# Kernel tuning notes

Measured on AMD Instinct MI355X. Metric: run time of the kernel, lower is better.

The kernel has to match this reference:

```python
import jax, jax.numpy as jnp
import numpy as np

B, C, H, W = 8, 128, 48, 48
RED = 16  # SELayer reduction


def setup_inputs() -> dict:
    key = jax.random.key(0)
    ks = jax.random.split(key, 8)
    s = 0.05  # weight scale for numerical stability of softmax
    return {
        "x": jax.random.normal(ks[0], (B, C, H, W), jnp.float32),
        "Wq": jax.random.normal(ks[1], (C, C), jnp.float32) * s,
        "bq": jnp.zeros((C,), jnp.float32),
        "Wk": jax.random.normal(ks[2], (C, C), jnp.float32) * s,
        "bk": jnp.zeros((C,), jnp.float32),
        "Wv": jax.random.normal(ks[3], (C, C), jnp.float32) * s,
        "bv": jnp.zeros((C,), jnp.float32),
        "se_w1": jax.random.normal(ks[4], (C // RED, C), jnp.float32) * s,
        "se_w2": jax.random.normal(ks[5], (C, C // RED), jnp.float32) * s,
        "gamma": jax.random.normal(ks[6], (1,), jnp.float32),
    }


def reference(x, Wq, bq, Wk, bk, Wv, bv, se_w1, se_w2, gamma):
    b, c, h, w = x.shape
    n = h * w
    xf = x.reshape(b, c, n)  # (B, C, N)
    # 1x1 convs == per-pixel linear maps over channels
    q = jnp.einsum('oc,bcn->bon', Wq, xf) + bq[None, :, None]  # (B, C, N)
    k = jnp.einsum('oc,bcn->bon', Wk, xf) + bk[None, :, None]
    v = jnp.einsum('oc,bcn->bon', Wv, xf) + bv[None, :, None]
    # energy[b, i, j] = sum_c q[b, c, i] * k[b, c, j]  (unscaled, as in source)
    energy = jnp.einsum('bci,bcj->bij', q, k)  # (B, N, N)
    attn = jax.nn.softmax(energy, axis=-1)
    # out[b, c, i] = sum_j v[b, c, j] * attn[b, i, j]
    out = jnp.einsum('bcj,bij->bci', v, attn).reshape(b, c, h, w)
    # SELayer applied to the input x
    y = jnp.mean(x, axis=(2, 3))  # (B, C) global average pool
    y = jax.nn.relu(y @ se_w1.T)  # (B, C//RED)
    y = jax.nn.sigmoid(y @ se_w2.T)  # (B, C)
    x_se = x * y[:, :, None, None]
    return gamma[0] * out + x_se
```

## Files before the change

kernel.cpp:

```cpp
#include <hip/hip_runtime.h>

typedef _Float16 half8 __attribute__((ext_vector_type(8)));
typedef _Float16 half4 __attribute__((ext_vector_type(4)));
typedef float f32x4 __attribute__((ext_vector_type(4)));

#define BATCH 8
#define CH 128
#define NPIX 2304
#define SPLIT 6
#define JTILES 6
#define BN (BATCH * NPIX)
#define LOG2E 1.44269504088896f
#define PB2 25.96851f

__device__ __forceinline__ f32x4 mfma32(half8 a, half8 b, f32x4 c) {
    return __builtin_amdgcn_mfma_f32_16x16x32_f16(a, b, c, 0, 0, 0);
}

__global__ __launch_bounds__(256) void k_prep(
        const float* __restrict__ x, const float* __restrict__ Wq,
        const float* __restrict__ Wk, const float* __restrict__ Wv,
        _Float16* __restrict__ Wh, float* __restrict__ y0) {
    const int bid = blockIdx.x;
    const int t = threadIdx.x;
    if (bid < 1024) {
        const int row = bid;
        const float4* p = (const float4*)(x + (size_t)row * NPIX);
        float s = 0.f;
        for (int tt = t; tt < NPIX / 4; tt += 256) {
            float4 v = p[tt];
            s += v.x + v.y + v.z + v.w;
        }
        for (int m = 1; m < 64; m <<= 1) s += __shfl_xor(s, m);
        __shared__ float ls[4];
        if ((t & 63) == 0) ls[t >> 6] = s;
        __syncthreads();
        if (t == 0) y0[row] = (ls[0] + ls[1] + ls[2] + ls[3]) * (1.0f / (float)NPIX);
    } else {
        int i = (bid - 1024) * 256 + t;
        const float* src = (i < 16384) ? Wq : ((i < 32768) ? Wk : Wv);
        Wh[i] = (_Float16)src[i & 16383];
    }
}

__global__ __launch_bounds__(256) void k_proj(
        const float* __restrict__ x, const _Float16* __restrict__ Wh,
        const float* __restrict__ bq, const float* __restrict__ bk, const float* __restrict__ bv,
        _Float16* __restrict__ qT, _Float16* __restrict__ kT, _Float16* __restrict__ vN,
        const float* __restrict__ y0, const float* __restrict__ se_w1,
        const float* __restrict__ se_w2, float* __restrict__ scale) {
    const int t = threadIdx.x;
    if (blockIdx.x == 72) {
        if (blockIdx.y != 0) return;
        __shared__ float ly[128];
        __shared__ float ly1[8];
        for (int b = 0; b < BATCH; ++b) {
            if (t < 128) ly[t] = y0[b * 128 + t];
            __syncthreads();
            if (t < 8) {
                float a = 0.f;
                for (int c = 0; c < 128; ++c) a += se_w1[t * 128 + c] * ly[c];
                ly1[t] = fmaxf(a, 0.f);
            }
            __syncthreads();
            if (t < 128) {
                float a = 0.f;
                for (int r = 0; r < 8; ++r) a += se_w2[t * 8 + r] * ly1[r];
                scale[b * 128 + t] = 1.f / (1.f + __expf(-a));
            }
            __syncthreads();
        }
        return;
    }

    const int n0 = blockIdx.x * 32;
    const int b = blockIdx.y;
    __shared__ __align__(16) _Float16 xt[32 * 128];
    __shared__ __align__(16) _Float16 ob[128 * 32];

    {
        const int c4 = (t & 31) * 4;
        const int nn = (t >> 5) * 4;
        const float* xb = x + (size_t)b * CH * NPIX + n0;
        float4 v0 = *(const float4*)(xb + (size_t)(c4 + 0) * NPIX + nn);
        float4 v1 = *(const float4*)(xb + (size_t)(c4 + 1) * NPIX + nn);
        float4 v2 = *(const float4*)(xb + (size_t)(c4 + 2) * NPIX + nn);
        float4 v3 = *(const float4*)(xb + (size_t)(c4 + 3) * NPIX + nn);
        const float xr[4][4] = {{v0.x, v1.x, v2.x, v3.x}, {v0.y, v1.y, v2.y, v3.y},
                                {v0.z, v1.z, v2.z, v3.z}, {v0.w, v1.w, v2.w, v3.w}};
        for (int i = 0; i < 4; ++i) {
            int n = nn + i;
            half4 h;
            h[0] = (_Float16)xr[i][0]; h[1] = (_Float16)xr[i][1];
            h[2] = (_Float16)xr[i][2]; h[3] = (_Float16)xr[i][3];
            *(half4*)(xt + n * 128 + (((c4 >> 3) ^ (n & 7)) * 8) + (c4 & 4)) = h;
        }
    }
    __syncthreads();

    const int lane = t & 63, w = t >> 6;
    const int ln15 = lane & 15, quad = lane >> 4;
    f32x4 zero4 = {0.f, 0.f, 0.f, 0.f};

    for (int proj = 0; proj < 3; ++proj) {
        const _Float16* W = Wh + proj * 16384;
        const float* bias = (proj == 0) ? bq : ((proj == 1) ? bk : bv);
        f32x4 acc[2][2];
        acc[0][0] = zero4; acc[0][1] = zero4; acc[1][0] = zero4; acc[1][1] = zero4;

        for (int kc = 0; kc < 4; ++kc) {
            half8 bf[2];
            for (int nt = 0; nt < 2; ++nt) {
                int n = nt * 16 + ln15;
                bf[nt] = *(const half8*)(xt + n * 128 + (((kc * 4 + quad) ^ (n & 7)) * 8));
            }
            for (int mt = 0; mt < 2; ++mt) {
                half8 af = *(const half8*)(W + (w * 32 + mt * 16 + ln15) * 128 + kc * 32 + quad * 8);
                acc[mt][0] = mfma32(af, bf[0], acc[mt][0]);
                acc[mt][1] = mfma32(af, bf[1], acc[mt][1]);
            }
        }
        __syncthreads();

        if (proj < 2) {
            for (int mt = 0; mt < 2; ++mt)
                for (int nt = 0; nt < 2; ++nt)
                    for (int r = 0; r < 4; ++r) {
                        int c = w * 32 + mt * 16 + quad * 4 + r;
                        int n = nt * 16 + ln15;
                        ob[n * 128 + (((c >> 3) ^ (n & 7)) * 8) + (c & 7)] =
                            (_Float16)(acc[mt][nt][r] + bias[c]);
                    }
            __syncthreads();
            _Float16* dst = ((proj == 0) ? qT : kT) + ((size_t)b * NPIX + n0) * CH;
            for (int rep = 0; rep < 2; ++rep) {
                int n = rep * 16 + (t >> 4), ch = t & 15;
                *(half8*)(dst + n * CH + ch * 8) =
                    *(const half8*)(ob + n * 128 + ((ch ^ (n & 7)) * 8));
            }
        } else {
            for (int mt = 0; mt < 2; ++mt)
                for (int nt = 0; nt < 2; ++nt)
                    for (int r = 0; r < 4; ++r) {
                        int c = w * 32 + mt * 16 + quad * 4 + r;
                        int n = nt * 16 + ln15;
                        ob[c * 32 + (((n >> 3) ^ (c & 3)) * 8) + (n & 7)] =
                            (_Float16)(acc[mt][nt][r] + bias[c]);
                    }
            __syncthreads();
            _Float16* vb = vN + (size_t)b * CH * NPIX + n0;
            for (int rep = 0; rep < 2; ++rep) {
                int c = rep * 64 + (t >> 2), ch = t & 3;
                *(half8*)(vb + (size_t)c * NPIX + ch * 8) =
                    *(const half8*)(ob + c * 32 + ((ch ^ (c & 3)) * 8));
            }
        }
    }
}

__global__ __launch_bounds__(256, 3) void k_attn(
        const _Float16* __restrict__ qT, const _Float16* __restrict__ kT,
        const _Float16* __restrict__ vN,
        _Float16* __restrict__ o_part, float* __restrict__ g_l) {
    const int i0 = blockIdx.x * 128;
    const int b = blockIdx.y;
    const int split = blockIdx.z;
    const int t = threadIdx.x;
    const int lane = t & 63, w = t >> 6;
    const int ln15 = lane & 15, quad = lane >> 4;

    __shared__ __align__(16) _Float16 sh[24576];
    _Float16* k_s = sh;
    _Float16* v_s = sh + 8192;
    _Float16* p_w = sh + 16384 + w * 2048;

    const int iA = i0 + w * 32 + ln15;
    half8 qfA[4], qfB[4];
    {
        const _Float16* qb = qT + ((size_t)b * NPIX + iA) * CH + quad * 8;
        for (int kc = 0; kc < 4; ++kc) {
            qfA[kc] = *(const half8*)(qb + kc * 32);
            qfB[kc] = *(const half8*)(qb + 16 * CH + kc * 32);
        }
    }

    f32x4 zero4 = {0.f, 0.f, 0.f, 0.f};
    f32x4 osA[8], osB[8];
    for (int ct = 0; ct < 8; ++ct) { osA[ct] = zero4; osB[ct] = zero4; }
    float lA = 0.f, lB = 0.f;

    const _Float16* kb = kT + ((size_t)b * NPIX + split * (JTILES * 64)) * CH;
    const _Float16* vb = vN + (size_t)b * CH * NPIX + split * (JTILES * 64);

    for (int it = 0; it < JTILES; ++it) {
        __syncthreads();
        {
            const _Float16* kk = kb + (size_t)it * 64 * CH;
            for (int rep = 0; rep < 4; ++rep) {
                int row = rep * 16 + (t >> 4), ch = t & 15;
                *(half8*)(k_s + row * 128 + ((ch ^ (row & 7)) * 8)) =
                    *(const half8*)(kk + row * CH + ch * 8);
            }
        }
        {
            const _Float16* vv = vb + it * 64;
            for (int rep = 0; rep < 4; ++rep) {
                int c = rep * 32 + (t >> 3), ch = t & 7;
                *(half8*)(v_s + c * 64 + ((ch ^ (c & 7)) * 8)) =
                    *(const half8*)(vv + (size_t)c * NPIX + ch * 8);
            }
        }
        __syncthreads();

        f32x4 sA[4], sB[4];
        for (int jt = 0; jt < 4; ++jt) { sA[jt] = zero4; sB[jt] = zero4; }
        for (int jt = 0; jt < 4; ++jt) {
            int row = jt * 16 + ln15;
            for (int kc = 0; kc < 4; ++kc) {
                half8 kf = *(const half8*)(k_s + row * 128 + (((kc * 4 + quad) ^ (row & 7)) * 8));
                sA[jt] = mfma32(kf, qfA[kc], sA[jt]);
                sB[jt] = mfma32(kf, qfB[kc], sB[jt]);
            }
        }

        {
            float sum = 0.f;
            for (int jt = 0; jt < 4; ++jt) {
                half4 ph;
                for (int r = 0; r < 4; ++r) {
                    float p = exp2f(fmaf(sA[jt][r], LOG2E, -PB2));
                    sum += p;
                    ph[r] = (_Float16)p;
                }
                *(half4*)(p_w + ln15 * 64 + (((jt * 4 + quad) ^ ln15) * 4)) = ph;
            }
            lA += sum;
        }
        {
            float sum = 0.f;
            for (int jt = 0; jt < 4; ++jt) {
                half4 ph;
                for (int r = 0; r < 4; ++r) {
                    float p = exp2f(fmaf(sB[jt][r], LOG2E, -PB2));
                    sum += p;
                    ph[r] = (_Float16)p;
                }
                *(half4*)(p_w + 1024 + ln15 * 64 + (((jt * 4 + quad) ^ ln15) * 4)) = ph;
            }
            lB += sum;
        }

        for (int t32 = 0; t32 < 2; ++t32) {
            int s0 = t32 * 8 + quad * 2;
            half4 a0 = *(const half4*)(p_w + ln15 * 64 + ((s0 ^ ln15) * 4));
            half4 a1 = *(const half4*)(p_w + ln15 * 64 + (((s0 + 1) ^ ln15) * 4));
            half4 b0 = *(const half4*)(p_w + 1024 + ln15 * 64 + ((s0 ^ ln15) * 4));
            half4 b1 = *(const half4*)(p_w + 1024 + ln15 * 64 + (((s0 + 1) ^ ln15) * 4));
            half8 pfA, pfB;
            for (int e = 0; e < 4; ++e) {
                pfA[e] = a0[e]; pfA[4 + e] = a1[e];
                pfB[e] = b0[e]; pfB[4 + e] = b1[e];
            }
            for (int ct = 0; ct < 8; ++ct) {
                int c = ct * 16 + ln15;
                half8 vf = *(const half8*)(v_s + c * 64 + (((t32 * 4 + quad) ^ (c & 7)) * 8));
                osA[ct] = mfma32(vf, pfA, osA[ct]);
                osB[ct] = mfma32(vf, pfB, osB[ct]);
            }
        }
    }

    lA += __shfl_xor(lA, 16); lA += __shfl_xor(lA, 32);
    lB += __shfl_xor(lB, 16); lB += __shfl_xor(lB, 32);
    if (quad == 0) {
        g_l[(size_t)(split * BATCH + b) * NPIX + iA] = lA;
        g_l[(size_t)(split * BATCH + b) * NPIX + iA + 16] = lB;
    }
    __syncthreads();
    for (int ct = 0; ct < 8; ++ct)
        for (int r = 0; r < 4; ++r) {
            int c = ct * 16 + quad * 4 + r;
            int il = w * 32 + ln15;
            sh[c * 128 + ((((il >> 3) ^ (c & 15)) * 8)) + (il & 7)] = (_Float16)osA[ct][r];
            int il2 = il + 16;
            sh[c * 128 + ((((il2 >> 3) ^ (c & 15)) * 8)) + (il2 & 7)] = (_Float16)osB[ct][r];
        }
    __syncthreads();
    _Float16* opb = o_part + (size_t)(split * BATCH + b) * CH * NPIX;
    for (int rep = 0; rep < 8; ++rep) {
        int c = rep * 16 + (t >> 4), ch = t & 15;
        *(half8*)(opb + (size_t)c * NPIX + i0 + ch * 8) =
            *(const half8*)(sh + c * 128 + ((ch ^ (c & 15)) * 8));
    }
}

__global__ __launch_bounds__(256) void k_combine(
        const _Float16* __restrict__ o_part, const float* __restrict__ g_l,
        const float* __restrict__ x, const float* __restrict__ scale,
        const float* __restrict__ gamma_p, float* __restrict__ out) {
    int tid = blockIdx.x * 256 + threadIdx.x;
    int i8 = (tid % (NPIX / 8)) * 8;
    int bc = tid / (NPIX / 8);
    int b = bc >> 7, c = bc & 127;

    float L[8] = {0.f, 0.f, 0.f, 0.f, 0.f, 0.f, 0.f, 0.f};
    for (int s = 0; s < SPLIT; ++s) {
        const float* lp = g_l + (size_t)(s * BATCH + b) * NPIX + i8;
        float4 la = *(const float4*)(lp);
        float4 lb = *(const float4*)(lp + 4);
        L[0] += la.x; L[1] += la.y; L[2] += la.z; L[3] += la.w;
        L[4] += lb.x; L[5] += lb.y; L[6] += lb.z; L[7] += lb.w;
    }
    float acc[8] = {0.f, 0.f, 0.f, 0.f, 0.f, 0.f, 0.f, 0.f};
    for (int s = 0; s < SPLIT; ++s) {
        half8 o = *(const half8*)(o_part + ((size_t)(s * BATCH + b) * CH + c) * NPIX + i8);
        for (int e = 0; e < 8; ++e) acc[e] += (float)o[e];
    }
    float g = gamma_p[0];
    float sc = scale[bc];
    size_t base = (size_t)bc * NPIX + i8;
    float4 x0 = *(const float4*)(x + base);
    float4 x1 = *(const float4*)(x + base + 4);
    float xv[8] = {x0.x, x0.y, x0.z, x0.w, x1.x, x1.y, x1.z, x1.w};
    float r[8];
    for (int e = 0; e < 8; ++e) r[e] = g * (acc[e] / L[e]) + xv[e] * sc;
    *(float4*)(out + base) = {r[0], r[1], r[2], r[3]};
    *(float4*)(out + base + 4) = {r[4], r[5], r[6], r[7]};
}

extern "C" void kernel_launch(void* const* d_in, const int* in_sizes, int n_in,
                              void* d_out, int out_size, void* d_ws, size_t ws_size,
                              hipStream_t stream) {
    const float* x     = (const float*)d_in[0];
    const float* Wq    = (const float*)d_in[1];
    const float* bq    = (const float*)d_in[2];
    const float* Wk    = (const float*)d_in[3];
    const float* bk    = (const float*)d_in[4];
    const float* Wv    = (const float*)d_in[5];
    const float* bv    = (const float*)d_in[6];
    const float* se_w1 = (const float*)d_in[7];
    const float* se_w2 = (const float*)d_in[8];
    const float* gamma = (const float*)d_in[9];
    float* out = (float*)d_out;

    char* ws = (char*)d_ws;
    const size_t E = (size_t)BATCH * NPIX * CH;
    _Float16* qT = (_Float16*)(ws);
    _Float16* kT = (_Float16*)(ws + E * 2);
    _Float16* vN = (_Float16*)(ws + E * 4);
    _Float16* op = (_Float16*)(ws + E * 6);
    char* tail   = ws + E * 6 + (size_t)SPLIT * E * 2;
    _Float16* Wh = (_Float16*)(tail);
    float* g_l   = (float*)(tail + 98304);
    float* y0    = (float*)(tail + 98304 + (size_t)SPLIT * BN * 4);
    float* scale = (float*)(tail + 98304 + (size_t)SPLIT * BN * 4 + 4096);

    k_prep<<<1216, 256, 0, stream>>>(x, Wq, Wk, Wv, Wh, y0);
    k_proj<<<dim3(73, BATCH), 256, 0, stream>>>(
        x, Wh, bq, bk, bv, qT, kT, vN, y0, se_w1, se_w2, scale);
    k_attn<<<dim3(NPIX / 128, BATCH, SPLIT), 256, 0, stream>>>(
        qT, kT, vN, op, g_l);
    k_combine<<<(int)(E / 8 / 256), 256, 0, stream>>>(
        op, g_l, x, scale, gamma, out);
}
```

Baseline: 178.7 us.

## Fold prep kernel into projection, split attention seven ways, shrink P staging

Removes the separate prep kernel. The global-average-pool sum is now computed inside the projection kernel with atomics, and the weights are converted from fp32 to fp16 on the fly. The SE MLP moves into the combine kernel, which recomputes it per block. Attention is split over 7 uneven j-ranges (6 or 5 tiles each) instead of 6, with smaller per-wave P staging so occupancy can rise to 4 blocks per CU. This trades one fewer launch and a larger grid for atomic contention, redundant SE work, and an extra memset launch.

```diff
diff --git a/kernel.cpp b/kernel.cpp
--- a/kernel.cpp
+++ b/kernel.cpp
@@ -7,8 +7,7 @@
 #define BATCH 8
 #define CH 128
 #define NPIX 2304
-#define SPLIT 6
-#define JTILES 6
+#define NSPLIT 7
 #define BN (BATCH * NPIX)
 #define LOG2E 1.44269504088896f
 #define PB2 25.96851f
@@ -17,64 +16,15 @@
     return __builtin_amdgcn_mfma_f32_16x16x32_f16(a, b, c, 0, 0, 0);
 }
 
-__global__ __launch_bounds__(256) void k_prep(
+__global__ __launch_bounds__(256) void k_proj(
         const float* __restrict__ x, const float* __restrict__ Wq,
         const float* __restrict__ Wk, const float* __restrict__ Wv,
-        _Float16* __restrict__ Wh, float* __restrict__ y0) {
-    const int bid = blockIdx.x;
-    const int t = threadIdx.x;
-    if (bid < 1024) {
-        const int row = bid;
-        const float4* p = (const float4*)(x + (size_t)row * NPIX);
-        float s = 0.f;
-        for (int tt = t; tt < NPIX / 4; tt += 256) {
-            float4 v = p[tt];
-            s += v.x + v.y + v.z + v.w;
-        }
-        for (int m = 1; m < 64; m <<= 1) s += __shfl_xor(s, m);
-        __shared__ float ls[4];
-        if ((t & 63) == 0) ls[t >> 6] = s;
-        __syncthreads();
-        if (t == 0) y0[row] = (ls[0] + ls[1] + ls[2] + ls[3]) * (1.0f / (float)NPIX);
-    } else {
-        int i = (bid - 1024) * 256 + t;
-        const float* src = (i < 16384) ? Wq : ((i < 32768) ? Wk : Wv);
-        Wh[i] = (_Float16)src[i & 16383];
-    }
-}
-
-__global__ __launch_bounds__(256) void k_proj(
-        const float* __restrict__ x, const _Float16* __restrict__ Wh,
         const float* __restrict__ bq, const float* __restrict__ bk, const float* __restrict__ bv,
         _Float16* __restrict__ qT, _Float16* __restrict__ kT, _Float16* __restrict__ vN,
-        const float* __restrict__ y0, const float* __restrict__ se_w1,
-        const float* __restrict__ se_w2, float* __restrict__ scale) {
-    const int t = threadIdx.x;
-    if (blockIdx.x == 72) {
-        if (blockIdx.y != 0) return;
-        __shared__ float ly[128];
-        __shared__ float ly1[8];
-        for (int b = 0; b < BATCH; ++b) {
-            if (t < 128) ly[t] = y0[b * 128 + t];
-            __syncthreads();
-            if (t < 8) {
-                float a = 0.f;
-                for (int c = 0; c < 128; ++c) a += se_w1[t * 128 + c] * ly[c];
-                ly1[t] = fmaxf(a, 0.f);
-            }
-            __syncthreads();
-            if (t < 128) {
-                float a = 0.f;
-                for (int r = 0; r < 8; ++r) a += se_w2[t * 8 + r] * ly1[r];
-                scale[b * 128 + t] = 1.f / (1.f + __expf(-a));
-            }
-            __syncthreads();
-        }
-        return;
-    }
-
+        float* __restrict__ y0) {
     const int n0 = blockIdx.x * 32;
     const int b = blockIdx.y;
+    const int t = threadIdx.x;
     __shared__ __align__(16) _Float16 xt[32 * 128];
     __shared__ __align__(16) _Float16 ob[128 * 32];
 
@@ -86,6 +36,11 @@
         float4 v1 = *(const float4*)(xb + (size_t)(c4 + 1) * NPIX + nn);
         float4 v2 = *(const float4*)(xb + (size_t)(c4 + 2) * NPIX + nn);
         float4 v3 = *(const float4*)(xb + (size_t)(c4 + 3) * NPIX + nn);
+        float ps[4] = {v0.x + v0.y + v0.z + v0.w, v1.x + v1.y + v1.z + v1.w,
+                       v2.x + v2.y + v2.z + v2.w, v3.x + v3.y + v3.z + v3.w};
+        for (int k = 0; k < 4; ++k) ps[k] += __shfl_xor(ps[k], 32);
+        if (((t >> 5) & 1) == 0)
+            for (int k = 0; k < 4; ++k) atomicAdd(&y0[b * 128 + c4 + k], ps[k]);
         const float xr[4][4] = {{v0.x, v1.x, v2.x, v3.x}, {v0.y, v1.y, v2.y, v3.y},
                                 {v0.z, v1.z, v2.z, v3.z}, {v0.w, v1.w, v2.w, v3.w}};
         for (int i = 0; i < 4; ++i) {
@@ -103,7 +58,7 @@
     f32x4 zero4 = {0.f, 0.f, 0.f, 0.f};
 
     for (int proj = 0; proj < 3; ++proj) {
-        const _Float16* W = Wh + proj * 16384;
+        const float* W = (proj == 0) ? Wq : ((proj == 1) ? Wk : Wv);
         const float* bias = (proj == 0) ? bq : ((proj == 1) ? bk : bv);
         f32x4 acc[2][2];
         acc[0][0] = zero4; acc[0][1] = zero4; acc[1][0] = zero4; acc[1][1] = zero4;
@@ -115,7 +70,14 @@
                 bf[nt] = *(const half8*)(xt + n * 128 + (((kc * 4 + quad) ^ (n & 7)) * 8));
             }
             for (int mt = 0; mt < 2; ++mt) {
-                half8 af = *(const half8*)(W + (w * 32 + mt * 16 + ln15) * 128 + kc * 32 + quad * 8);
+                const float* wr = W + (w * 32 + mt * 16 + ln15) * 128 + kc * 32 + quad * 8;
+                float4 wa = *(const float4*)(wr);
+                float4 wb = *(const float4*)(wr + 4);
+                half8 af;
+                af[0] = (_Float16)wa.x; af[1] = (_Float16)wa.y;
+                af[2] = (_Float16)wa.z; af[3] = (_Float16)wa.w;
+                af[4] = (_Float16)wb.x; af[5] = (_Float16)wb.y;
+                af[6] = (_Float16)wb.z; af[7] = (_Float16)wb.w;
                 acc[mt][0] = mfma32(af, bf[0], acc[mt][0]);
                 acc[mt][1] = mfma32(af, bf[1], acc[mt][1]);
             }
@@ -158,21 +120,23 @@
     }
 }
 
-__global__ __launch_bounds__(256, 3) void k_attn(
+__global__ __launch_bounds__(256, 4) void k_attn(
         const _Float16* __restrict__ qT, const _Float16* __restrict__ kT,
         const _Float16* __restrict__ vN,
         _Float16* __restrict__ o_part, float* __restrict__ g_l) {
     const int i0 = blockIdx.x * 128;
     const int b = blockIdx.y;
     const int split = blockIdx.z;
+    const int tiles = (split == 0) ? 6 : 5;
+    const int jb = (split == 0) ? 0 : (1 + split * 5);
     const int t = threadIdx.x;
     const int lane = t & 63, w = t >> 6;
     const int ln15 = lane & 15, quad = lane >> 4;
 
-    __shared__ __align__(16) _Float16 sh[24576];
+    __shared__ __align__(16) _Float16 sh[20480];
     _Float16* k_s = sh;
     _Float16* v_s = sh + 8192;
-    _Float16* p_w = sh + 16384 + w * 2048;
+    _Float16* p_w = sh + 16384 + w * 1024;
 
     const int iA = i0 + w * 32 + ln15;
     half8 qfA[4], qfB[4];
@@ -189,10 +153,10 @@
     for (int ct = 0; ct < 8; ++ct) { osA[ct] = zero4; osB[ct] = zero4; }
     float lA = 0.f, lB = 0.f;
 
-    const _Float16* kb = kT + ((size_t)b * NPIX + split * (JTILES * 64)) * CH;
-    const _Float16* vb = vN + (size_t)b * CH * NPIX + split * (JTILES * 64);
-
-    for (int it = 0; it < JTILES; ++it) {
+    const _Float16* kb = kT + ((size_t)b * NPIX + jb * 64) * CH;
+    const _Float16* vb = vN + (size_t)b * CH * NPIX + jb * 64;
+
+    for (int it = 0; it < tiles; ++it) {
         __syncthreads();
         {
             const _Float16* kk = kb + (size_t)it * 64 * CH;
@@ -223,39 +187,29 @@
             }
         }
 
+        half4 phA[4], phB[4];
         {
-            float sum = 0.f;
-            for (int jt = 0; jt < 4; ++jt) {
-                half4 ph;
+            float sumA = 0.f, sumB = 0.f;
+            for (int jt = 0; jt < 4; ++jt)
                 for (int r = 0; r < 4; ++r) {
-                    float p = exp2f(fmaf(sA[jt][r], LOG2E, -PB2));
-                    sum += p;
-                    ph[r] = (_Float16)p;
+                    float pa = exp2f(fmaf(sA[jt][r], LOG2E, -PB2));
+                    float pb = exp2f(fmaf(sB[jt][r], LOG2E, -PB2));
+                    sumA += pa; sumB += pb;
+                    phA[jt][r] = (_Float16)pa; phB[jt][r] = (_Float16)pb;
                 }
-                *(half4*)(p_w + ln15 * 64 + (((jt * 4 + quad) ^ ln15) * 4)) = ph;
-            }
-            lA += sum;
-        }
-        {
-            float sum = 0.f;
-            for (int jt = 0; jt < 4; ++jt) {
-                half4 ph;
-                for (int r = 0; r < 4; ++r) {
-                    float p = exp2f(fmaf(sB[jt][r], LOG2E, -PB2));
-                    sum += p;
-                    ph[r] = (_Float16)p;
-                }
-                *(half4*)(p_w + 1024 + ln15 * 64 + (((jt * 4 + quad) ^ ln15) * 4)) = ph;
-            }
-            lB += sum;
-        }
-
-        for (int t32 = 0; t32 < 2; ++t32) {
-            int s0 = t32 * 8 + quad * 2;
-            half4 a0 = *(const half4*)(p_w + ln15 * 64 + ((s0 ^ ln15) * 4));
-            half4 a1 = *(const half4*)(p_w + ln15 * 64 + (((s0 + 1) ^ ln15) * 4));
-            half4 b0 = *(const half4*)(p_w + 1024 + ln15 * 64 + ((s0 ^ ln15) * 4));
-            half4 b1 = *(const half4*)(p_w + 1024 + ln15 * 64 + (((s0 + 1) ^ ln15) * 4));
+            lA += sumA; lB += sumB;
+        }
+
+        for (int h = 0; h < 2; ++h) {
+            for (int u = 0; u < 2; ++u) {
+                int slot = u * 4 + quad;
+                *(half4*)(p_w + ln15 * 32 + ((slot ^ (ln15 & 7)) * 4)) = phA[2 * h + u];
+                *(half4*)(p_w + 512 + ln15 * 32 + ((slot ^ (ln15 & 7)) * 4)) = phB[2 * h + u];
+            }
+            half4 a0 = *(const half4*)(p_w + ln15 * 32 + (((quad * 2 + 0) ^ (ln15 & 7)) * 4));
+            half4 a1 = *(const half4*)(p_w + ln15 * 32 + (((quad * 2 + 1) ^ (ln15 & 7)) * 4));
+            half4 b0 = *(const half4*)(p_w + 512 + ln15 * 32 + (((quad * 2 + 0) ^ (ln15 & 7)) * 4));
+            half4 b1 = *(const half4*)(p_w + 512 + ln15 * 32 + (((quad * 2 + 1) ^ (ln15 & 7)) * 4));
             half8 pfA, pfB;
             for (int e = 0; e < 4; ++e) {
                 pfA[e] = a0[e]; pfA[4 + e] = a1[e];
@@ -263,7 +217,7 @@
             }
             for (int ct = 0; ct < 8; ++ct) {
                 int c = ct * 16 + ln15;
-                half8 vf = *(const half8*)(v_s + c * 64 + (((t32 * 4 + quad) ^ (c & 7)) * 8));
+                half8 vf = *(const half8*)(v_s + c * 64 + (((h * 4 + quad) ^ (c & 7)) * 8));
                 osA[ct] = mfma32(vf, pfA, osA[ct]);
                 osB[ct] = mfma32(vf, pfB, osB[ct]);
             }
@@ -296,15 +250,48 @@
 
 __global__ __launch_bounds__(256) void k_combine(
         const _Float16* __restrict__ o_part, const float* __restrict__ g_l,
-        const float* __restrict__ x, const float* __restrict__ scale,
+        const float* __restrict__ x, const float* __restrict__ y0,
+        const float* __restrict__ se_w1, const float* __restrict__ se_w2,
         const float* __restrict__ gamma_p, float* __restrict__ out) {
-    int tid = blockIdx.x * 256 + threadIdx.x;
+    const int t = threadIdx.x;
+    const int tid = blockIdx.x * 256 + t;
+    const int bc0 = (blockIdx.x * 256) / 288;
+
+    __shared__ float part[2][2][8];
+    __shared__ float sc_s[2];
+    {
+        int pair = t >> 7;
+        int bcx = min(bc0 + pair, BATCH * CH - 1);
+        int bb = bcx >> 7;
+        int cl = t & 127;
+        float yv = y0[bb * 128 + cl] * (1.0f / (float)NPIX);
+        float pr[8];
+        for (int r = 0; r < 8; ++r) pr[r] = se_w1[r * 128 + cl] * yv;
+        for (int r = 0; r < 8; ++r)
+            for (int m = 1; m < 64; m <<= 1) pr[r] += __shfl_xor(pr[r], m);
+        if ((t & 63) == 0)
+            for (int r = 0; r < 8; ++r) part[pair][(t >> 6) & 1][r] = pr[r];
+    }
+    __syncthreads();
+    if (t < 2) {
+        int bcx = min(bc0 + t, BATCH * CH - 1);
+        int cx = bcx & 127;
+        float a = 0.f;
+        for (int r = 0; r < 8; ++r) {
+            float y1 = fmaxf(part[t][0][r] + part[t][1][r], 0.f);
+            a += se_w2[cx * 8 + r] * y1;
+        }
+        sc_s[t] = 1.f / (1.f + __expf(-a));
+    }
+    __syncthreads();
+
     int i8 = (tid % (NPIX / 8)) * 8;
     int bc = tid / (NPIX / 8);
     int b = bc >> 7, c = bc & 127;
+    float sc = sc_s[bc - bc0];
 
     float L[8] = {0.f, 0.f, 0.f, 0.f, 0.f, 0.f, 0.f, 0.f};
-    for (int s = 0; s < SPLIT; ++s) {
+    for (int s = 0; s < NSPLIT; ++s) {
         const float* lp = g_l + (size_t)(s * BATCH + b) * NPIX + i8;
         float4 la = *(const float4*)(lp);
         float4 lb = *(const float4*)(lp + 4);
@@ -312,12 +299,11 @@
         L[4] += lb.x; L[5] += lb.y; L[6] += lb.z; L[7] += lb.w;
     }
     float acc[8] = {0.f, 0.f, 0.f, 0.f, 0.f, 0.f, 0.f, 0.f};
-    for (int s = 0; s < SPLIT; ++s) {
+    for (int s = 0; s < NSPLIT; ++s) {
         half8 o = *(const half8*)(o_part + ((size_t)(s * BATCH + b) * CH + c) * NPIX + i8);
         for (int e = 0; e < 8; ++e) acc[e] += (float)o[e];
     }
     float g = gamma_p[0];
-    float sc = scale[bc];
     size_t base = (size_t)bc * NPIX + i8;
     float4 x0 = *(const float4*)(x + base);
     float4 x1 = *(const float4*)(x + base + 4);
@@ -349,17 +335,15 @@
     _Float16* kT = (_Float16*)(ws + E * 2);
     _Float16* vN = (_Float16*)(ws + E * 4);
     _Float16* op = (_Float16*)(ws + E * 6);
-    char* tail   = ws + E * 6 + (size_t)SPLIT * E * 2;
-    _Float16* Wh = (_Float16*)(tail);
-    float* g_l   = (float*)(tail + 98304);
-    float* y0    = (float*)(tail + 98304 + (size_t)SPLIT * BN * 4);
-    float* scale = (float*)(tail + 98304 + (size_t)SPLIT * BN * 4 + 4096);
-
-    k_prep<<<1216, 256, 0, stream>>>(x, Wq, Wk, Wv, Wh, y0);
-    k_proj<<<dim3(73, BATCH), 256, 0, stream>>>(
-        x, Wh, bq, bk, bv, qT, kT, vN, y0, se_w1, se_w2, scale);
-    k_attn<<<dim3(NPIX / 128, BATCH, SPLIT), 256, 0, stream>>>(
+    char* tail   = ws + E * 6 + (size_t)NSPLIT * E * 2;
+    float* g_l   = (float*)(tail);
+    float* y0    = (float*)(tail + (size_t)NSPLIT * BN * 4);
+
+    hipMemsetAsync(y0, 0, BATCH * CH * sizeof(float), stream);
+    k_proj<<<dim3(72, BATCH), 256, 0, stream>>>(
+        x, Wq, Wk, Wv, bq, bk, bv, qT, kT, vN, y0);
+    k_attn<<<dim3(NPIX / 128, BATCH, NSPLIT), 256, 0, stream>>>(
         qT, kT, vN, op, g_l);
     k_combine<<<(int)(E / 8 / 256), 256, 0, stream>>>(
-        op, g_l, x, scale, gamma, out);
-}
+        op, g_l, x, y0, se_w1, se_w2, gamma, out);
+}
```

After: 235.2 us. +31.6%, slower.
